# Kernel optimization log

Measured on AMD Instinct MI355X. Metric: run time of the kernel, lower is better.

## Reference

```python
import jax, jax.numpy as jnp
import numpy as np

EMBED = 256; HEADS = 8; LEVELS = 4; POINTS = 4; HID = 1024
HD = EMBED // HEADS
SHAPES = [(100, 100), (50, 50), (25, 25), (13, 13)]
STARTS = [0]
for _h, _w in SHAPES[:-1]:
    STARTS.append(STARTS[-1] + _h * _w)
TOTAL = sum(h * w for h, w in SHAPES)
BS = 2
EPS = 1e-5


def _ln(x, g, b):
    m = x.mean(-1, keepdims=True)
    v = ((x - m) ** 2).mean(-1, keepdims=True)
    return (x - m) / jnp.sqrt(v + EPS) * g + b


def _msda(query, value, ref, norm_wh, params):
    W_value, b_value, W_off, b_off, W_attn, b_attn, W_out, b_out = params
    bs, T, _ = query.shape
    v = (value @ W_value + b_value).reshape(bs, T, HEADS, HD)
    v = jnp.moveaxis(v, 2, 1)  # [bs, H, T, hd]
    off = (query @ W_off + b_off).reshape(bs, T, HEADS, LEVELS, POINTS, 2)
    aw = (query @ W_attn + b_attn).reshape(bs, T, HEADS, LEVELS * POINTS)
    aw = jax.nn.softmax(aw, axis=-1).reshape(bs, T, HEADS, LEVELS, POINTS)
    aw = jnp.moveaxis(aw, 2, 1)  # [bs, H, T, L, P]
    # sampling locations in [0,1] coords: ref + offset / (W_l, H_l)
    loc = ref[:, :, None, :, None, :] + off / norm_wh[None, None, None, :, None, :]
    loc = jnp.moveaxis(loc, 2, 1)  # [bs, H, T, L, P, 2]
    out = jnp.zeros((bs, HEADS, T, HD), query.dtype)
    for l, (Hl, Wl) in enumerate(SHAPES):
        s = STARTS[l]
        v_l = v[:, :, s:s + Hl * Wl]  # [bs, H, HW_l, hd]
        # grid_sample(align_corners=False): pixel = loc * size - 0.5
        x = loc[:, :, :, l, :, 0] * Wl - 0.5  # [bs, H, T, P]
        y = loc[:, :, :, l, :, 1] * Hl - 0.5
        x0 = jnp.floor(x); y0 = jnp.floor(y)
        wx1 = x - x0; wy1 = y - y0
        x0i = x0.astype(jnp.int32); y0i = y0.astype(jnp.int32)

        def samp(xi, yi):
            valid = (xi >= 0) & (xi < Wl) & (yi >= 0) & (yi < Hl)
            idx = jnp.clip(yi, 0, Hl - 1) * Wl + jnp.clip(xi, 0, Wl - 1)
            idx = idx.reshape(bs, HEADS, -1)
            g = jnp.take_along_axis(v_l, idx[..., None], axis=2)
            g = g.reshape(bs, HEADS, T, POINTS, HD)
            return g * valid[..., None].astype(g.dtype)

        bil = ((1 - wy1) * (1 - wx1))[..., None] * samp(x0i, y0i) \
            + ((1 - wy1) * wx1)[..., None] * samp(x0i + 1, y0i) \
            + (wy1 * (1 - wx1))[..., None] * samp(x0i, y0i + 1) \
            + (wy1 * wx1)[..., None] * samp(x0i + 1, y0i + 1)
        out = out + (bil * aw[:, :, :, l, :, None]).sum(axis=3)
    out = jnp.moveaxis(out, 1, 2).reshape(bs, T, EMBED)
    return out @ W_out + b_out


def setup_inputs() -> dict:
    key = jax.random.key(0)
    ks = jax.random.split(key, 16)
    s = 0.02
    f32 = jnp.float32
    return {
        "src": jax.random.normal(ks[0], (BS, TOTAL, EMBED), f32),
        "pos": jax.random.normal(ks[1], (BS, TOTAL, EMBED), f32),
        "reference_points": jax.random.uniform(ks[2], (BS, TOTAL, LEVELS, 2), f32),
        "spatial_shapes": jnp.array(SHAPES, jnp.int32),
        "level_start_index": jnp.array(STARTS, jnp.int32),
        "ln1_g": jnp.ones((EMBED,), f32), "ln1_b": jnp.zeros((EMBED,), f32),
        "ln2_g": jnp.ones((EMBED,), f32), "ln2_b": jnp.zeros((EMBED,), f32),
        "W_value": jax.random.normal(ks[3], (EMBED, EMBED), f32) * s,
        "b_value": jnp.zeros((EMBED,), f32),
        "W_off": jax.random.normal(ks[4], (EMBED, HEADS * LEVELS * POINTS * 2), f32) * s,
        "b_off": jax.random.normal(ks[5], (HEADS * LEVELS * POINTS * 2,), f32) * 0.5,
        "W_attn": jax.random.normal(ks[6], (EMBED, HEADS * LEVELS * POINTS), f32) * s,
        "b_attn": jnp.zeros((HEADS * LEVELS * POINTS,), f32),
        "W_out": jax.random.normal(ks[7], (EMBED, EMBED), f32) * s,
        "b_out": jnp.zeros((EMBED,), f32),
        "W_ffn1": jax.random.normal(ks[8], (EMBED, HID), f32) * s,
        "b_ffn1": jnp.zeros((HID,), f32),
        "W_ffn2": jax.random.normal(ks[9], (HID, EMBED), f32) * s,
        "b_ffn2": jnp.zeros((EMBED,), f32),
    }


def reference(src, pos, reference_points, spatial_shapes, level_start_index,
              ln1_g, ln1_b, ln2_g, ln2_b,
              W_value, b_value, W_off, b_off, W_attn, b_attn, W_out, b_out,
              W_ffn1, b_ffn1, W_ffn2, b_ffn2):
    src_n = _ln(src, ln1_g, ln1_b)
    q = src_n + pos
    # offset normalizer is (W_l, H_l)
    norm_wh = jnp.stack([spatial_shapes[:, 1], spatial_shapes[:, 0]], -1).astype(src.dtype)
    attn = _msda(q, src_n, reference_points, norm_wh,
                 (W_value, b_value, W_off, b_off, W_attn, b_attn, W_out, b_out))
    src1 = src + attn  # dropout = identity (eval)
    src_n2 = _ln(src1, ln2_g, ln2_b)
    ffn = jax.nn.relu(src_n2 @ W_ffn1 + b_ffn1) @ W_ffn2 + b_ffn2
    return src1 + ffn
```

## Files before the change

kernel.cpp:

```cpp
#include <hip/hip_runtime.h>
#include <hip/hip_bf16.h>

#define T_TOK   13294
#define BS_     2
#define M_ROWS  (BS_ * T_TOK)
#define EMBED_  256
#define HID_    1024

typedef __attribute__((ext_vector_type(8))) short short8;
typedef __attribute__((ext_vector_type(4))) float f32x4;

__device__ __forceinline__ unsigned short f2bf(float f) {
  __hip_bfloat16 h = __float2bfloat16(f);
  return *reinterpret_cast<unsigned short*>(&h);
}
__device__ __forceinline__ float bf2f(unsigned short u) {
  unsigned int x = ((unsigned int)u) << 16;
  return __uint_as_float(x);
}

__global__ __launch_bounds__(256) void prep_kernel(
    const float* __restrict__ s0, const float* __restrict__ s1,
    const float* __restrict__ s2, const float* __restrict__ s3,
    const float* __restrict__ s4, const float* __restrict__ s5,
    unsigned short* __restrict__ d0, unsigned short* __restrict__ d1,
    unsigned short* __restrict__ d2, unsigned short* __restrict__ d3,
    unsigned short* __restrict__ d4, unsigned short* __restrict__ d5,
    const float* __restrict__ x, const float* __restrict__ pos,
    const float* __restrict__ g, const float* __restrict__ bta,
    unsigned short* __restrict__ y, unsigned short* __restrict__ q) {
  const int bid = blockIdx.x;
  if (bid < 736) {
    __shared__ float t[32][33];
    const float* S; unsigned short* D; int K, N, t0;
    if      (bid <  64) { S = s0; D = d0; K = 256;  N = 256;  t0 = 0;   }
    else if (bid < 128) { S = s1; D = d1; K = 256;  N = 256;  t0 = 64;  }
    else if (bid < 160) { S = s2; D = d2; K = 256;  N = 128;  t0 = 128; }
    else if (bid < 224) { S = s3; D = d3; K = 256;  N = 256;  t0 = 160; }
    else if (bid < 480) { S = s4; D = d4; K = 256;  N = 1024; t0 = 224; }
    else                { S = s5; D = d5; K = 1024; N = 256;  t0 = 480; }
    const int tile = bid - t0;
    const int ntx = N >> 5;
    const int k0 = (tile / ntx) * 32, n0 = (tile % ntx) * 32;
    const int tx = threadIdx.x & 31, ty = threadIdx.x >> 5;
    #pragma unroll
    for (int i = 0; i < 32; i += 8)
      t[ty + i][tx] = S[(size_t)(k0 + ty + i) * N + n0 + tx];
    __syncthreads();
    #pragma unroll
    for (int i = 0; i < 32; i += 8)
      D[(size_t)(n0 + ty + i) * K + k0 + tx] = f2bf(t[tx][ty + i]);
    return;
  }
  const int wave = threadIdx.x >> 6, lane = threadIdx.x & 63;
  const int r = (bid - 736) * 4 + wave;
  if (r >= M_ROWS) return;
  const size_t base = (size_t)r * 256 + lane * 4;
  const float4 v = *reinterpret_cast<const float4*>(&x[base]);

  float lsum = v.x + v.y + v.z + v.w;
  #pragma unroll
  for (int m = 32; m; m >>= 1) lsum += __shfl_xor(lsum, m, 64);
  const float mean = lsum * (1.0f / 256.0f);

  const float dx = v.x - mean, dy = v.y - mean, dz = v.z - mean, dw = v.w - mean;
  float lsq = dx * dx + dy * dy + dz * dz + dw * dw;
  #pragma unroll
  for (int m = 32; m; m >>= 1) lsq += __shfl_xor(lsq, m, 64);
  const float rinv = rsqrtf(lsq * (1.0f / 256.0f) + 1e-5f);

  const float4 gg = *reinterpret_cast<const float4*>(&g[lane * 4]);
  const float4 bb = *reinterpret_cast<const float4*>(&bta[lane * 4]);
  const float o0 = dx * rinv * gg.x + bb.x;
  const float o1 = dy * rinv * gg.y + bb.y;
  const float o2 = dz * rinv * gg.z + bb.z;
  const float o3 = dw * rinv * gg.w + bb.w;
  ushort4 yo; yo.x = f2bf(o0); yo.y = f2bf(o1); yo.z = f2bf(o2); yo.w = f2bf(o3);
  *reinterpret_cast<ushort4*>(&y[base]) = yo;
  const float4 pp = *reinterpret_cast<const float4*>(&pos[base]);
  ushort4 qo;
  qo.x = f2bf(o0 + pp.x); qo.y = f2bf(o1 + pp.y);
  qo.z = f2bf(o2 + pp.z); qo.w = f2bf(o3 + pp.w);
  *reinterpret_cast<ushort4*>(&q[base]) = qo;
}

template <int K>
__device__ __forceinline__ void stage64(
    const unsigned short* __restrict__ A, const unsigned short* __restrict__ Wt,
    unsigned short* As, unsigned short* Bs,
    int M, int row0, int col0, int k0, int lane) {
  #pragma unroll
  for (int i = 0; i < 4; ++i) {
    const int chunk = i * 64 + lane;
    const int rrow = chunk >> 2;
    const int kgs = (chunk & 3) ^ ((rrow >> 1) & 3);
    int ga = row0 + rrow; if (ga >= M) ga = M - 1;
    __builtin_amdgcn_global_load_lds(
        (const __attribute__((address_space(1))) void*)(A + (size_t)ga * K + k0 + kgs * 8),
        (__attribute__((address_space(3))) void*)(As + chunk * 8), 16, 0, 0);
  }
  #pragma unroll
  for (int i = 0; i < 4; ++i) {
    const int chunk = i * 64 + lane;
    const int rrow = chunk >> 2;
    const int kgs = (chunk & 3) ^ ((rrow >> 1) & 3);
    __builtin_amdgcn_global_load_lds(
        (const __attribute__((address_space(1))) void*)(Wt + (size_t)(col0 + rrow) * K + k0 + kgs * 8),
        (__attribute__((address_space(3))) void*)(Bs + chunk * 8), 16, 0, 0);
  }
}

template <int EPI, bool OUTBF, int K>
__device__ __forceinline__ void wgemm_core(
    const unsigned short* __restrict__ A, const unsigned short* __restrict__ Wt,
    const float* __restrict__ bias, const float* __restrict__ R,
    void* __restrict__ Cv, void* __restrict__ Cv2,
    int M, int N, int row0, int col0, unsigned short* lds) {
  const int lane = threadIdx.x & 63;
  unsigned short* As = lds;
  unsigned short* Bs = lds + 64 * 32;

  f32x4 acc[4][4] = {};
  const int frow = lane & 15;
  const int fke = ((lane >> 4) ^ ((frow >> 1) & 3)) * 8;

  stage64<K>(A, Wt, As, Bs, M, row0, col0, 0, lane);
  asm volatile("s_waitcnt vmcnt(0)" ::: "memory");

  #pragma unroll
  for (int k0 = 0; k0 < K; k0 += 32) {
    short8 a[4], b[4];
    #pragma unroll
    for (int mi = 0; mi < 4; ++mi)
      a[mi] = *reinterpret_cast<const short8*>(&As[(mi * 16 + frow) * 32 + fke]);
    #pragma unroll
    for (int ni = 0; ni < 4; ++ni)
      b[ni] = *reinterpret_cast<const short8*>(&Bs[(ni * 16 + frow) * 32 + fke]);
    asm volatile("s_waitcnt lgkmcnt(0)" ::: "memory");
    __builtin_amdgcn_sched_barrier(0);

    if (k0 + 32 < K)
      stage64<K>(A, Wt, As, Bs, M, row0, col0, k0 + 32, lane);

    #pragma unroll
    for (int mi = 0; mi < 4; ++mi)
      #pragma unroll
      for (int ni = 0; ni < 4; ++ni)
        acc[mi][ni] = __builtin_amdgcn_mfma_f32_16x16x32_bf16(b[ni], a[mi], acc[mi][ni], 0, 0, 0);

    if (k0 + 32 < K)
      asm volatile("s_waitcnt vmcnt(0)" ::: "memory");
  }

  const int lr = lane & 15;
  const int cb = (lane >> 4) * 4;
  #pragma unroll
  for (int mi = 0; mi < 4; ++mi) {
    const int grow = row0 + mi * 16 + lr;
    if (grow >= M) continue;
    #pragma unroll
    for (int ni = 0; ni < 4; ++ni) {
      const int gcol = col0 + ni * 16 + cb;
      float4 b4;
      if (EPI == 3) b4 = (gcol < 256) ? *reinterpret_cast<const float4*>(&bias[gcol])
                                      : *reinterpret_cast<const float4*>(&R[gcol - 256]);
      else          b4 = *reinterpret_cast<const float4*>(&bias[gcol]);
      float v0 = acc[mi][ni][0] + b4.x;
      float v1 = acc[mi][ni][1] + b4.y;
      float v2 = acc[mi][ni][2] + b4.z;
      float v3 = acc[mi][ni][3] + b4.w;
      if (EPI == 1) {
        v0 = fmaxf(v0, 0.f); v1 = fmaxf(v1, 0.f);
        v2 = fmaxf(v2, 0.f); v3 = fmaxf(v3, 0.f);
      }
      if (EPI == 2) {
        const float4 r4 = *reinterpret_cast<const float4*>(&R[(size_t)grow * N + gcol]);
        v0 += r4.x; v1 += r4.y; v2 += r4.z; v3 += r4.w;
        float4 o; o.x = v0; o.y = v1; o.z = v2; o.w = v3;
        *reinterpret_cast<float4*>(&((float*)Cv)[(size_t)grow * N + gcol]) = o;
      } else if (EPI == 4) {
        const unsigned short* Rb = (const unsigned short*)R;
        const ushort4 r4 = *reinterpret_cast<const ushort4*>(&Rb[(size_t)grow * N + gcol]);
        v0 += bf2f(r4.x); v1 += bf2f(r4.y); v2 += bf2f(r4.z); v3 += bf2f(r4.w);
        float4 o; o.x = v0; o.y = v1; o.z = v2; o.w = v3;
        *reinterpret_cast<float4*>(&((float*)Cv)[(size_t)grow * N + gcol]) = o;
      } else {
        ushort4 o;
        o.x = f2bf(v0); o.y = f2bf(v1); o.z = f2bf(v2); o.w = f2bf(v3);
        if (EPI == 3) {
          if (gcol < 256)
            *reinterpret_cast<ushort4*>(&((unsigned short*)Cv )[(size_t)grow * 256 + gcol]) = o;
          else
            *reinterpret_cast<ushort4*>(&((unsigned short*)Cv2)[(size_t)grow * 128 + gcol - 256]) = o;
        } else {
          *reinterpret_cast<ushort4*>(&((unsigned short*)Cv)[(size_t)grow * N + gcol]) = o;
        }
      }
    }
  }
}

template <int EPI, bool OUTBF, int K>
__global__ __launch_bounds__(256, 3) void wgemm_k(
    const unsigned short* __restrict__ A, const unsigned short* __restrict__ Wt,
    const float* __restrict__ bias, const float* __restrict__ R,
    void* __restrict__ Cv, int M, int N) {
  __shared__ unsigned short lds[4 * 4096];
  const int w = threadIdx.x >> 6;
  const int nwg = gridDim.x;
  const int bid = blockIdx.x;
  const int wgid = (bid & 7) * (nwg >> 3) + (bid >> 3);
  const int tile = wgid * 4 + w;
  const int CT = N >> 6;
  const int row0 = (tile / CT) * 64;
  const int col0 = (tile % CT) * 64;
  wgemm_core<EPI, OUTBF, K>(A, Wt, bias, R, Cv, nullptr, M, N, row0, col0,
                            lds + w * 4096);
}

__global__ __launch_bounds__(256, 3) void wproj_fused(
    const unsigned short* __restrict__ srcn, const unsigned short* __restrict__ q,
    const unsigned short* __restrict__ wt_val, const unsigned short* __restrict__ wt_offattn,
    const float* __restrict__ b_value, const float* __restrict__ b_off,
    const float* __restrict__ b_attn,
    unsigned short* __restrict__ vout, unsigned short* __restrict__ offout,
    unsigned short* __restrict__ awout, int M) {
  __shared__ unsigned short lds[4 * 4096];
  const int w = threadIdx.x >> 6;
  const int nwg = gridDim.x;
  const int bid = blockIdx.x;
  const int wgid = (bid & 7) * (nwg >> 3) + (bid >> 3);
  const int tile = wgid * 4 + w;
  if (tile < 1664) {
    const int row0 = (tile >> 2) * 64, col0 = (tile & 3) * 64;
    wgemm_core<0, true, 256>(srcn, wt_val, b_value, nullptr, vout, nullptr,
                             M, 256, row0, col0, lds + w * 4096);
  } else {
    const int t2 = tile - 1664;
    const int row0 = (t2 / 6) * 64, col0 = (t2 % 6) * 64;
    wgemm_core<3, false, 256>(q, wt_offattn, b_off, b_attn, offout, awout,
                              M, 384, row0, col0, lds + w * 4096);
  }
}

__global__ __launch_bounds__(256, 3) void outln_kernel(
    const unsigned short* __restrict__ attn, const unsigned short* __restrict__ wt_out,
    const float* __restrict__ b_out, const float* __restrict__ src,
    const float* __restrict__ ln_g, const float* __restrict__ ln_b,
    unsigned short* __restrict__ src1, unsigned short* __restrict__ sn2, int M) {
  __shared__ unsigned short lds[4 * 4096];
  __shared__ float s_sum[64][4];
  __shared__ float s_sq[64][4];
  const int w = threadIdx.x >> 6, lane = threadIdx.x & 63;
  const int nwg = gridDim.x;
  const int bid = blockIdx.x;
  const int wgid = (bid & 7) * (nwg >> 3) + (bid >> 3);
  const int row0 = wgid * 64;
  const int col0 = w * 64;
  unsigned short* As = lds + w * 4096;
  unsigned short* Bs = As + 64 * 32;

  f32x4 acc[4][4] = {};
  const int frow = lane & 15;
  const int fke = ((lane >> 4) ^ ((frow >> 1) & 3)) * 8;

  stage64<256>(attn, wt_out, As, Bs, M, row0, col0, 0, lane);
  asm volatile("s_waitcnt vmcnt(0)" ::: "memory");
  #pragma unroll
  for (int k0 = 0; k0 < 256; k0 += 32) {
    short8 a[4], b[4];
    #pragma unroll
    for (int mi = 0; mi < 4; ++mi)
      a[mi] = *reinterpret_cast<const short8*>(&As[(mi * 16 + frow) * 32 + fke]);
    #pragma unroll
    for (int ni = 0; ni < 4; ++ni)
      b[ni] = *reinterpret_cast<const short8*>(&Bs[(ni * 16 + frow) * 32 + fke]);
    asm volatile("s_waitcnt lgkmcnt(0)" ::: "memory");
    __builtin_amdgcn_sched_barrier(0);
    if (k0 + 32 < 256)
      stage64<256>(attn, wt_out, As, Bs, M, row0, col0, k0 + 32, lane);
    #pragma unroll
    for (int mi = 0; mi < 4; ++mi)
      #pragma unroll
      for (int ni = 0; ni < 4; ++ni)
        acc[mi][ni] = __builtin_amdgcn_mfma_f32_16x16x32_bf16(b[ni], a[mi], acc[mi][ni], 0, 0, 0);
    if (k0 + 32 < 256)
      asm volatile("s_waitcnt vmcnt(0)" ::: "memory");
  }

  const int lr = lane & 15;
  const int cb = (lane >> 4) * 4;
  float lsum[4], lsq[4];
  #pragma unroll
  for (int mi = 0; mi < 4; ++mi) {
    const int grow = row0 + mi * 16 + lr;
    const bool ok = grow < M;
    float rs = 0.f, rq = 0.f;
    #pragma unroll
    for (int ni = 0; ni < 4; ++ni) {
      const int gcol = col0 + ni * 16 + cb;
      const float4 b4 = *reinterpret_cast<const float4*>(&b_out[gcol]);
      float4 r4 = make_float4(0.f, 0.f, 0.f, 0.f);
      if (ok) r4 = *reinterpret_cast<const float4*>(&src[(size_t)grow * 256 + gcol]);
      float v0 = acc[mi][ni][0] + b4.x + r4.x;
      float v1 = acc[mi][ni][1] + b4.y + r4.y;
      float v2 = acc[mi][ni][2] + b4.z + r4.z;
      float v3 = acc[mi][ni][3] + b4.w + r4.w;
      acc[mi][ni][0] = v0; acc[mi][ni][1] = v1;
      acc[mi][ni][2] = v2; acc[mi][ni][3] = v3;
      if (ok) {
        ushort4 o;
        o.x = f2bf(v0); o.y = f2bf(v1); o.z = f2bf(v2); o.w = f2bf(v3);
        *reinterpret_cast<ushort4*>(&src1[(size_t)grow * 256 + gcol]) = o;
      }
      rs += v0 + v1 + v2 + v3;
      rq += v0 * v0 + v1 * v1 + v2 * v2 + v3 * v3;
    }
    lsum[mi] = rs; lsq[mi] = rq;
  }
  #pragma unroll
  for (int mi = 0; mi < 4; ++mi) {
    lsum[mi] += __shfl_xor(lsum[mi], 16, 64);
    lsum[mi] += __shfl_xor(lsum[mi], 32, 64);
    lsq[mi]  += __shfl_xor(lsq[mi], 16, 64);
    lsq[mi]  += __shfl_xor(lsq[mi], 32, 64);
  }
  if (lane < 16) {
    #pragma unroll
    for (int mi = 0; mi < 4; ++mi) {
      s_sum[mi * 16 + lane][w] = lsum[mi];
      s_sq[mi * 16 + lane][w] = lsq[mi];
    }
  }
  __syncthreads();
  #pragma unroll
  for (int mi = 0; mi < 4; ++mi) {
    const int lrow = mi * 16 + lr;
    const int grow = row0 + lrow;
    if (grow >= M) continue;
    const float ssum = s_sum[lrow][0] + s_sum[lrow][1] + s_sum[lrow][2] + s_sum[lrow][3];
    const float ssq = s_sq[lrow][0] + s_sq[lrow][1] + s_sq[lrow][2] + s_sq[lrow][3];
    const float mean = ssum * (1.0f / 256.0f);
    const float var = ssq * (1.0f / 256.0f) - mean * mean;
    const float rinv = rsqrtf(var + 1e-5f);
    #pragma unroll
    for (int ni = 0; ni < 4; ++ni) {
      const int gcol = col0 + ni * 16 + cb;
      const float4 g4 = *reinterpret_cast<const float4*>(&ln_g[gcol]);
      const float4 bb = *reinterpret_cast<const float4*>(&ln_b[gcol]);
      ushort4 o;
      o.x = f2bf((acc[mi][ni][0] - mean) * rinv * g4.x + bb.x);
      o.y = f2bf((acc[mi][ni][1] - mean) * rinv * g4.y + bb.y);
      o.z = f2bf((acc[mi][ni][2] - mean) * rinv * g4.z + bb.z);
      o.w = f2bf((acc[mi][ni][3] - mean) * rinv * g4.w + bb.w);
      *reinterpret_cast<ushort4*>(&sn2[(size_t)grow * 256 + gcol]) = o;
    }
  }
}

__global__ __launch_bounds__(256) void msda_kernel(
    const unsigned short* __restrict__ v, const unsigned short* __restrict__ offb,
    const unsigned short* __restrict__ awl, const float* __restrict__ ref,
    unsigned short* __restrict__ outb) {
  const int r0 = blockIdx.x * 8;
  const int tid = threadIdx.x;

  __shared__ float s_aw[8 * 128];
  __shared__ float s_ref[64];
  __shared__ float2 s_wi[64 * 66];

  if (tid < 64) {
    int rr = r0 + (tid >> 3); if (rr >= M_ROWS) rr = M_ROWS - 1;
    s_ref[tid] = ref[(size_t)rr * 8 + (tid & 7)];
  }

  {
    const int g = tid >> 2, j = tid & 3;
    const int tok = g >> 3, h = g & 7;
    int rr = r0 + tok; if (rr >= M_ROWS) rr = M_ROWS - 1;
    const uint2 u = *reinterpret_cast<const uint2*>(&awl[(size_t)rr * 128 + h * 16 + j * 4]);
    const float l0 = bf2f((unsigned short)(u.x & 0xffff));
    const float l1 = bf2f((unsigned short)(u.x >> 16));
    const float l2 = bf2f((unsigned short)(u.y & 0xffff));
    const float l3 = bf2f((unsigned short)(u.y >> 16));
    float mx = fmaxf(fmaxf(l0, l1), fmaxf(l2, l3));
    mx = fmaxf(mx, __shfl_xor(mx, 1, 64));
    mx = fmaxf(mx, __shfl_xor(mx, 2, 64));
    const float e0 = expf(l0 - mx), e1 = expf(l1 - mx);
    const float e2 = expf(l2 - mx), e3 = expf(l3 - mx);
    float ss = e0 + e1 + e2 + e3;
    ss += __shfl_xor(ss, 1, 64);
    ss += __shfl_xor(ss, 2, 64);
    const float inv = 1.0f / ss;
    float4 w4; w4.x = e0 * inv; w4.y = e1 * inv; w4.z = e2 * inv; w4.w = e3 * inv;
    *reinterpret_cast<float4*>(&s_aw[g * 16 + j * 4]) = w4;
  }
  __syncthreads();

  const int HH[4] = {100, 50, 25, 13};
  const int WW[4] = {100, 50, 25, 13};
  const int SS[4] = {0, 10000, 12500, 13125};

  {
    const int pi0 = tid * 4;
    const int tok = pi0 >> 7, h = (pi0 >> 4) & 7;
    const int g = pi0 >> 4;
    const int pt0 = pi0 & 15;
    const int l = pt0 >> 2;
    int rr = r0 + tok; if (rr >= M_ROWS) rr = M_ROWS - 1;
    const float Wl = (float)WW[l], Hl = (float)HH[l];
    const float rx = s_ref[tok * 8 + l * 2], ry = s_ref[tok * 8 + l * 2 + 1];
    const uint4 uoff = *reinterpret_cast<const uint4*>(&offb[(size_t)rr * 256 + h * 32 + pt0 * 2]);
    const float4 aw4 = *reinterpret_cast<const float4*>(&s_aw[g * 16 + pt0]);
    const unsigned int uo[4] = {uoff.x, uoff.y, uoff.z, uoff.w};
    const float awv[4] = {aw4.x, aw4.y, aw4.z, aw4.w};
    #pragma unroll
    for (int p = 0; p < 4; ++p) {
      const float ox = bf2f((unsigned short)(uo[p] & 0xffff));
      const float oy = bf2f((unsigned short)(uo[p] >> 16));
      const float x = rx * Wl + ox - 0.5f;
      const float y = ry * Hl + oy - 0.5f;
      const float x0f = floorf(x), y0f = floorf(y);
      const int x0 = (int)x0f, y0 = (int)y0f;
      const float wx1 = x - x0f, wy1 = y - y0f;
      const float wx0 = 1.f - wx1, wy0 = 1.f - wy1;
      const float aw = awv[p];
      #pragma unroll
      for (int c = 0; c < 4; ++c) {
        const int xx = x0 + (c & 1), yy = y0 + (c >> 1);
        const bool valid = (xx >= 0) & (xx < WW[l]) & (yy >= 0) & (yy < HH[l]);
        const int xc = min(max(xx, 0), WW[l] - 1);
        const int yc = min(max(yy, 0), HH[l] - 1);
        float wgt = aw * ((c & 1) ? wx1 : wx0) * ((c >> 1) ? wy1 : wy0);
        wgt = valid ? wgt : 0.f;
        const int idxb = (SS[l] + yc * WW[l] + xc) * 512;
        s_wi[g * 66 + (pt0 + p) * 4 + c] = make_float2(wgt, __int_as_float(idxb));
      }
    }
  }
  __syncthreads();

  const int tok = tid >> 5;
  const int h = (tid >> 2) & 7;
  const int d8 = tid & 3;
  const int r = r0 + tok;
  const int rc = (r < M_ROWS) ? r : M_ROWS - 1;
  const int b = rc / T_TOK;
  const char* vb = (const char*)(v + (size_t)b * T_TOK * 256 + h * 32 + d8 * 8);
  const int e0 = (tok * 8 + h) * 66;

  float a0 = 0.f, a1 = 0.f, a2 = 0.f, a3 = 0.f;
  float a4 = 0.f, a5 = 0.f, a6 = 0.f, a7 = 0.f;
  #pragma unroll 8
  for (int j = 0; j < 64; ++j) {
    const float2 wi = s_wi[e0 + j];
    const float wgt = wi.x;
    const int idxb = __float_as_int(wi.y);
    const uint4 u = *reinterpret_cast<const uint4*>(vb + idxb);
    a0 = fmaf(wgt, bf2f((unsigned short)(u.x & 0xffff)), a0);
    a1 = fmaf(wgt, bf2f((unsigned short)(u.x >> 16)), a1);
    a2 = fmaf(wgt, bf2f((unsigned short)(u.y & 0xffff)), a2);
    a3 = fmaf(wgt, bf2f((unsigned short)(u.y >> 16)), a3);
    a4 = fmaf(wgt, bf2f((unsigned short)(u.z & 0xffff)), a4);
    a5 = fmaf(wgt, bf2f((unsigned short)(u.z >> 16)), a5);
    a6 = fmaf(wgt, bf2f((unsigned short)(u.w & 0xffff)), a6);
    a7 = fmaf(wgt, bf2f((unsigned short)(u.w >> 16)), a7);
  }
  if (r < M_ROWS) {
    uint4 o;
    o.x = ((unsigned int)f2bf(a0)) | ((unsigned int)f2bf(a1) << 16);
    o.y = ((unsigned int)f2bf(a2)) | ((unsigned int)f2bf(a3) << 16);
    o.z = ((unsigned int)f2bf(a4)) | ((unsigned int)f2bf(a5) << 16);
    o.w = ((unsigned int)f2bf(a6)) | ((unsigned int)f2bf(a7) << 16);
    *reinterpret_cast<uint4*>(&outb[(size_t)r * 256 + h * 32 + d8 * 8]) = o;
  }
}

extern "C" void kernel_launch(void* const* d_in, const int* in_sizes, int n_in,
                              void* d_out, int out_size, void* d_ws, size_t ws_size,
                              hipStream_t stream) {
  const float* src     = (const float*)d_in[0];
  const float* pos     = (const float*)d_in[1];
  const float* ref     = (const float*)d_in[2];
  const float* ln1_g   = (const float*)d_in[5];
  const float* ln1_b   = (const float*)d_in[6];
  const float* ln2_g   = (const float*)d_in[7];
  const float* ln2_b   = (const float*)d_in[8];
  const float* W_value = (const float*)d_in[9];
  const float* b_value = (const float*)d_in[10];
  const float* W_off   = (const float*)d_in[11];
  const float* b_off   = (const float*)d_in[12];
  const float* W_attn  = (const float*)d_in[13];
  const float* b_attn  = (const float*)d_in[14];
  const float* W_out   = (const float*)d_in[15];
  const float* b_out   = (const float*)d_in[16];
  const float* W_ffn1  = (const float*)d_in[17];
  const float* b_ffn1  = (const float*)d_in[18];
  const float* W_ffn2  = (const float*)d_in[19];
  const float* b_ffn2  = (const float*)d_in[20];
  float* out = (float*)d_out;

  const int M = M_ROWS;
  const size_t n256 = (size_t)M * 256;

  unsigned short* src_n_bf = (unsigned short*)d_ws;
  unsigned short* q_bf     = src_n_bf + n256;
  unsigned short* v_bf     = q_bf + n256;
  unsigned short* attn_bf  = v_bf + n256;
  unsigned short* sn2_bf   = attn_bf + n256;
  unsigned short* hid_bf   = sn2_bf + n256;
  unsigned short* offb     = hid_bf + (size_t)M * 1024;
  unsigned short* awbuf    = offb + n256;
  unsigned short* src1_bf  = awbuf + (size_t)M * 128;
  unsigned short* wt_val     = src1_bf + n256;
  unsigned short* wt_offattn = wt_val + 256 * 256;
  unsigned short* wt_out     = wt_offattn + 384 * 256;
  unsigned short* wt_ffn1    = wt_out + 256 * 256;
  unsigned short* wt_ffn2    = wt_ffn1 + 1024 * 256;

  prep_kernel<<<736 + (M + 3) / 4, 256, 0, stream>>>(
      W_value, W_off, W_attn, W_out, W_ffn1, W_ffn2,
      wt_val, wt_offattn, wt_offattn + 256 * 256, wt_out, wt_ffn1, wt_ffn2,
      src, pos, ln1_g, ln1_b, src_n_bf, q_bf);

  wproj_fused<<<1040, 256, 0, stream>>>(
      src_n_bf, q_bf, wt_val, wt_offattn, b_value, b_off, b_attn,
      v_bf, offb, awbuf, M);

  msda_kernel<<<(M + 7) / 8, 256, 0, stream>>>(v_bf, offb, awbuf, ref, attn_bf);

  outln_kernel<<<416, 256, 0, stream>>>(attn_bf, wt_out, b_out, src,
                                        ln2_g, ln2_b, src1_bf, sn2_bf, M);

  wgemm_k<1, true, 256 ><<<1664, 256, 0, stream>>>(sn2_bf, wt_ffn1, b_ffn1, nullptr,
                                                   hid_bf, M, 1024);
  wgemm_k<4, false, 1024><<<416, 256, 0, stream>>>(hid_bf, wt_ffn2, b_ffn2,
                                                   (const float*)src1_bf,
                                                   out, M, 256);
}
```

Measured before the change: 187.1 us.

## Use single-wave 64-thread GEMM blocks with 64-deep K staging

The weight-projection and FFN GEMMs switch from 256-thread blocks holding four independent per-wave tiles to 64-thread blocks that each own one 64x64 tile. Each K step now stages 64 elements instead of 32, using an 8-way XOR swizzle, and splits into two MFMA halves so the next stage's loads overlap the second half. This halves the number of load/wait rounds and gives the scheduler finer-grained blocks. The cost is twice the LDS per wave and many more small workgroups, which affects occupancy and dispatch overhead.

```diff
diff --git a/kernel.cpp b/kernel.cpp
--- a/kernel.cpp
+++ b/kernel.cpp
@@ -110,48 +110,37 @@
   }
 }
 
-template <int EPI, bool OUTBF, int K>
-__device__ __forceinline__ void wgemm_core(
+template <int K>
+__device__ __forceinline__ void stage64x64(
     const unsigned short* __restrict__ A, const unsigned short* __restrict__ Wt,
-    const float* __restrict__ bias, const float* __restrict__ R,
+    unsigned short* As, unsigned short* Bs,
+    int M, int row0, int col0, int k0, int lane) {
+  #pragma unroll
+  for (int i = 0; i < 8; ++i) {
+    const int chunk = i * 64 + lane;
+    const int rrow = chunk >> 3;
+    const int kgs = (chunk & 7) ^ (rrow & 7);
+    int ga = row0 + rrow; if (ga >= M) ga = M - 1;
+    __builtin_amdgcn_global_load_lds(
+        (const __attribute__((address_space(1))) void*)(A + (size_t)ga * K + k0 + kgs * 8),
+        (__attribute__((address_space(3))) void*)(As + chunk * 8), 16, 0, 0);
+  }
+  #pragma unroll
+  for (int i = 0; i < 8; ++i) {
+    const int chunk = i * 64 + lane;
+    const int rrow = chunk >> 3;
+    const int kgs = (chunk & 7) ^ (rrow & 7);
+    __builtin_amdgcn_global_load_lds(
+        (const __attribute__((address_space(1))) void*)(Wt + (size_t)(col0 + rrow) * K + k0 + kgs * 8),
+        (__attribute__((address_space(3))) void*)(Bs + chunk * 8), 16, 0, 0);
+  }
+}
+
+template <int EPI, bool OUTBF>
+__device__ __forceinline__ void gemm_epilogue(
+    f32x4 (&acc)[4][4], const float* __restrict__ bias, const float* __restrict__ R,
     void* __restrict__ Cv, void* __restrict__ Cv2,
-    int M, int N, int row0, int col0, unsigned short* lds) {
-  const int lane = threadIdx.x & 63;
-  unsigned short* As = lds;
-  unsigned short* Bs = lds + 64 * 32;
-
-  f32x4 acc[4][4] = {};
-  const int frow = lane & 15;
-  const int fke = ((lane >> 4) ^ ((frow >> 1) & 3)) * 8;
-
-  stage64<K>(A, Wt, As, Bs, M, row0, col0, 0, lane);
-  asm volatile("s_waitcnt vmcnt(0)" ::: "memory");
-
-  #pragma unroll
-  for (int k0 = 0; k0 < K; k0 += 32) {
-    short8 a[4], b[4];
-    #pragma unroll
-    for (int mi = 0; mi < 4; ++mi)
-      a[mi] = *reinterpret_cast<const short8*>(&As[(mi * 16 + frow) * 32 + fke]);
-    #pragma unroll
-    for (int ni = 0; ni < 4; ++ni)
-      b[ni] = *reinterpret_cast<const short8*>(&Bs[(ni * 16 + frow) * 32 + fke]);
-    asm volatile("s_waitcnt lgkmcnt(0)" ::: "memory");
-    __builtin_amdgcn_sched_barrier(0);
-
-    if (k0 + 32 < K)
-      stage64<K>(A, Wt, As, Bs, M, row0, col0, k0 + 32, lane);
-
-    #pragma unroll
-    for (int mi = 0; mi < 4; ++mi)
-      #pragma unroll
-      for (int ni = 0; ni < 4; ++ni)
-        acc[mi][ni] = __builtin_amdgcn_mfma_f32_16x16x32_bf16(b[ni], a[mi], acc[mi][ni], 0, 0, 0);
-
-    if (k0 + 32 < K)
-      asm volatile("s_waitcnt vmcnt(0)" ::: "memory");
-  }
-
+    int M, int N, int row0, int col0, int lane) {
   const int lr = lane & 15;
   const int cb = (lane >> 4) * 4;
   #pragma unroll
@@ -201,45 +190,106 @@
 }
 
 template <int EPI, bool OUTBF, int K>
-__global__ __launch_bounds__(256, 3) void wgemm_k(
+__device__ __forceinline__ void wgemm64_core(
+    const unsigned short* __restrict__ A, const unsigned short* __restrict__ Wt,
+    const float* __restrict__ bias, const float* __restrict__ R,
+    void* __restrict__ Cv, void* __restrict__ Cv2,
+    int M, int N, int row0, int col0, unsigned short* lds) {
+  const int lane = threadIdx.x & 63;
+  unsigned short* As = lds;
+  unsigned short* Bs = lds + 64 * 64;
+
+  f32x4 acc[4][4] = {};
+  const int frow = lane & 15;
+  const int gsel = lane >> 4;
+
+  stage64x64<K>(A, Wt, As, Bs, M, row0, col0, 0, lane);
+  asm volatile("s_waitcnt vmcnt(0)" ::: "memory");
+
+  #pragma unroll
+  for (int k0 = 0; k0 < K; k0 += 64) {
+    short8 a0[4], b0[4];
+    #pragma unroll
+    for (int mi = 0; mi < 4; ++mi) {
+      const int r = mi * 16 + frow;
+      a0[mi] = *reinterpret_cast<const short8*>(&As[r * 64 + ((gsel ^ (r & 7)) * 8)]);
+    }
+    #pragma unroll
+    for (int ni = 0; ni < 4; ++ni) {
+      const int r = ni * 16 + frow;
+      b0[ni] = *reinterpret_cast<const short8*>(&Bs[r * 64 + ((gsel ^ (r & 7)) * 8)]);
+    }
+    #pragma unroll
+    for (int mi = 0; mi < 4; ++mi)
+      #pragma unroll
+      for (int ni = 0; ni < 4; ++ni)
+        acc[mi][ni] = __builtin_amdgcn_mfma_f32_16x16x32_bf16(b0[ni], a0[mi], acc[mi][ni], 0, 0, 0);
+
+    short8 a1[4], b1[4];
+    #pragma unroll
+    for (int mi = 0; mi < 4; ++mi) {
+      const int r = mi * 16 + frow;
+      a1[mi] = *reinterpret_cast<const short8*>(&As[r * 64 + (((4 + gsel) ^ (r & 7)) * 8)]);
+    }
+    #pragma unroll
+    for (int ni = 0; ni < 4; ++ni) {
+      const int r = ni * 16 + frow;
+      b1[ni] = *reinterpret_cast<const short8*>(&Bs[r * 64 + (((4 + gsel) ^ (r & 7)) * 8)]);
+    }
+    asm volatile("s_waitcnt lgkmcnt(0)" ::: "memory");
+    __builtin_amdgcn_sched_barrier(0);
+
+    if (k0 + 64 < K)
+      stage64x64<K>(A, Wt, As, Bs, M, row0, col0, k0 + 64, lane);
+
+    #pragma unroll
+    for (int mi = 0; mi < 4; ++mi)
+      #pragma unroll
+      for (int ni = 0; ni < 4; ++ni)
+        acc[mi][ni] = __builtin_amdgcn_mfma_f32_16x16x32_bf16(b1[ni], a1[mi], acc[mi][ni], 0, 0, 0);
+
+    if (k0 + 64 < K)
+      asm volatile("s_waitcnt vmcnt(0)" ::: "memory");
+  }
+
+  gemm_epilogue<EPI, OUTBF>(acc, bias, R, Cv, Cv2, M, N, row0, col0, lane);
+}
+
+template <int EPI, bool OUTBF, int K>
+__global__ __launch_bounds__(64) void wgemm64_k(
     const unsigned short* __restrict__ A, const unsigned short* __restrict__ Wt,
     const float* __restrict__ bias, const float* __restrict__ R,
     void* __restrict__ Cv, int M, int N) {
-  __shared__ unsigned short lds[4 * 4096];
-  const int w = threadIdx.x >> 6;
+  __shared__ unsigned short lds[2 * 64 * 64];
   const int nwg = gridDim.x;
   const int bid = blockIdx.x;
   const int wgid = (bid & 7) * (nwg >> 3) + (bid >> 3);
-  const int tile = wgid * 4 + w;
   const int CT = N >> 6;
-  const int row0 = (tile / CT) * 64;
-  const int col0 = (tile % CT) * 64;
-  wgemm_core<EPI, OUTBF, K>(A, Wt, bias, R, Cv, nullptr, M, N, row0, col0,
-                            lds + w * 4096);
-}
-
-__global__ __launch_bounds__(256, 3) void wproj_fused(
+  const int row0 = (wgid / CT) * 64;
+  const int col0 = (wgid % CT) * 64;
+  wgemm64_core<EPI, OUTBF, K>(A, Wt, bias, R, Cv, nullptr, M, N, row0, col0, lds);
+}
+
+__global__ __launch_bounds__(64) void wproj64_fused(
     const unsigned short* __restrict__ srcn, const unsigned short* __restrict__ q,
     const unsigned short* __restrict__ wt_val, const unsigned short* __restrict__ wt_offattn,
     const float* __restrict__ b_value, const float* __restrict__ b_off,
     const float* __restrict__ b_attn,
     unsigned short* __restrict__ vout, unsigned short* __restrict__ offout,
     unsigned short* __restrict__ awout, int M) {
-  __shared__ unsigned short lds[4 * 4096];
-  const int w = threadIdx.x >> 6;
+  __shared__ unsigned short lds[2 * 64 * 64];
   const int nwg = gridDim.x;
   const int bid = blockIdx.x;
-  const int wgid = (bid & 7) * (nwg >> 3) + (bid >> 3);
-  const int tile = wgid * 4 + w;
+  const int tile = (bid & 7) * (nwg >> 3) + (bid >> 3);
   if (tile < 1664) {
     const int row0 = (tile >> 2) * 64, col0 = (tile & 3) * 64;
-    wgemm_core<0, true, 256>(srcn, wt_val, b_value, nullptr, vout, nullptr,
-                             M, 256, row0, col0, lds + w * 4096);
+    wgemm64_core<0, true, 256>(srcn, wt_val, b_value, nullptr, vout, nullptr,
+                               M, 256, row0, col0, lds);
   } else {
     const int t2 = tile - 1664;
     const int row0 = (t2 / 6) * 64, col0 = (t2 % 6) * 64;
-    wgemm_core<3, false, 256>(q, wt_offattn, b_off, b_attn, offout, awout,
-                              M, 384, row0, col0, lds + w * 4096);
+    wgemm64_core<3, false, 256>(q, wt_offattn, b_off, b_attn, offout, awout,
+                                M, 384, row0, col0, lds);
   }
 }
 
@@ -523,7 +573,7 @@
       wt_val, wt_offattn, wt_offattn + 256 * 256, wt_out, wt_ffn1, wt_ffn2,
       src, pos, ln1_g, ln1_b, src_n_bf, q_bf);
 
-  wproj_fused<<<1040, 256, 0, stream>>>(
+  wproj64_fused<<<4160, 64, 0, stream>>>(
       src_n_bf, q_bf, wt_val, wt_offattn, b_value, b_off, b_attn,
       v_bf, offb, awbuf, M);
 
@@ -532,9 +582,9 @@
   outln_kernel<<<416, 256, 0, stream>>>(attn_bf, wt_out, b_out, src,
                                         ln2_g, ln2_b, src1_bf, sn2_bf, M);
 
-  wgemm_k<1, true, 256 ><<<1664, 256, 0, stream>>>(sn2_bf, wt_ffn1, b_ffn1, nullptr,
-                                                   hid_bf, M, 1024);
-  wgemm_k<4, false, 1024><<<416, 256, 0, stream>>>(hid_bf, wt_ffn2, b_ffn2,
-                                                   (const float*)src1_bf,
-                                                   out, M, 256);
-}
+  wgemm64_k<1, true, 256 ><<<6656, 64, 0, stream>>>(sn2_bf, wt_ffn1, b_ffn1, nullptr,
+                                                    hid_bf, M, 1024);
+  wgemm64_k<4, false, 1024><<<1664, 64, 0, stream>>>(hid_bf, wt_ffn2, b_ffn2,
+                                                     (const float*)src1_bf,
+                                                     out, M, 256);
+}
```

Measured after the change: 175.5 us, median of 2. -6.2%, faster.
